# Optimization experiments

Hardware: AMD Instinct MI355X
Metric: run time of the kernel (lower is better)

The kernel has to match this reference:

```python
import jax, jax.numpy as jnp
from jax import lax
import numpy as np

B, T = 64, 256
V_CHAR, V_DICT = 8000, 30
CHAR_E, POS_E = 256, 128
POS_H, MAIN_H = 256, 512      # bidirectional output dims
LBL = 18 + 2                  # label_size + START/STOP


def _lstm_dir(x, maskf, Wih, Whh, b):
    """Unidirectional LSTM with PyTorch gate order (i,f,g,o); masked steps hold state, outputs zeroed at pads."""
    Bb = x.shape[0]
    H = Whh.shape[1]
    def step(carry, inp):
        h, c = carry
        xt, mt = inp  # xt [B,D], mt [B,1]
        g = xt @ Wih.T + h @ Whh.T + b
        i, f, gg, o = jnp.split(g, 4, axis=-1)
        c2 = jax.nn.sigmoid(f) * c + jax.nn.sigmoid(i) * jnp.tanh(gg)
        h2 = jax.nn.sigmoid(o) * jnp.tanh(c2)
        h = mt * h2 + (1.0 - mt) * h
        c = mt * c2 + (1.0 - mt) * c
        return (h, c), h * mt
    init = (jnp.zeros((Bb, H), x.dtype), jnp.zeros((Bb, H), x.dtype))
    _, ys = lax.scan(step, init, (x.transpose(1, 0, 2), maskf.T[:, :, None]))
    return ys.transpose(1, 0, 2)  # [B,T,H]


def _bilstm(x, lengths, maskf, Wih_f, Whh_f, b_f, Wih_b, Whh_b, b_b):
    """Packed-sequence BiLSTM: backward direction runs over each sequence reversed by its own length."""
    Tt = x.shape[1]
    out_f = _lstm_dir(x, maskf, Wih_f, Whh_f, b_f)
    rev_idx = jnp.clip(lengths[:, None] - 1 - jnp.arange(Tt)[None, :], 0, Tt - 1)  # [B,T]
    x_rev = jnp.take_along_axis(x, rev_idx[:, :, None], axis=1)
    out_b_rev = _lstm_dir(x_rev, maskf, Wih_b, Whh_b, b_b)
    out_b = jnp.take_along_axis(out_b_rev, rev_idx[:, :, None], axis=1) * maskf[:, :, None]
    return jnp.concatenate([out_f, out_b], axis=-1)


def _viterbi(emit, mask, trans):
    """CRF Viterbi decode. emit [B,T,L], mask [B,T] bool, trans [L,L] (trans[i,j]=score i->j); START=L-2, STOP=L-1."""
    Bb, Tt, L = emit.shape
    START, STOP = L - 2, L - 1
    alpha0 = trans[START][None, :] + emit[:, 0]  # [B,L]
    ident = jnp.arange(L)[None, :]
    def step(alpha, inp):
        e_t, m_t = inp  # [B,L], [B,1]
        scores = alpha[:, :, None] + trans[None, :, :]  # [B,L_prev,L_cur]
        bp = jnp.argmax(scores, axis=1)
        new = jnp.max(scores, axis=1) + e_t
        alpha = jnp.where(m_t, new, alpha)
        bp = jnp.where(m_t, bp, ident)
        return alpha, bp
    alpha, bps = lax.scan(step, alpha0, (emit[:, 1:].transpose(1, 0, 2), mask[:, 1:].T[:, :, None]))
    final = alpha + trans[:, STOP][None, :]
    last_tag = jnp.argmax(final, axis=1)          # [B]
    path_score = jnp.max(final, axis=1)           # [B]
    def back(tag, bp_t):
        prev = jnp.take_along_axis(bp_t, tag[:, None], axis=1)[:, 0]
        return prev, tag
    first_tag, tags_rest = lax.scan(back, last_tag, bps, reverse=True)  # tags_rest [T-1,B]
    tags = jnp.concatenate([first_tag[:, None], tags_rest.T], axis=1)   # [B,T]
    return path_score, tags * mask.astype(tags.dtype)


def setup_inputs() -> dict:
    key = jax.random.key(0)
    ks = jax.random.split(key, 24)
    char_inputs = jax.random.randint(ks[0], (B, T), 0, V_CHAR)
    pos_inputs = jax.random.randint(ks[1], (B, T), 0, V_DICT)
    tag_inputs = jax.random.randint(ks[2], (B, T), 0, V_DICT)
    lengths = jnp.sort(jax.random.randint(ks[3], (B,), T // 2, T + 1))[::-1]
    lengths = lengths.at[0].set(T)  # pack_padded requires descending lengths; max len defines T
    mask = jnp.arange(T)[None, :] < lengths[:, None]
    s = 0.08
    def rn(k, shape):
        return jax.random.normal(k, shape, jnp.float32) * s
    Hp, Hm = POS_H // 2, MAIN_H // 2
    Dm = CHAR_E + POS_E + POS_H
    return dict(
        char_inputs=char_inputs, pos_inputs=pos_inputs, tag_inputs=tag_inputs,
        lengths=lengths, mask=mask,
        char_emb=rn(ks[4], (V_CHAR, CHAR_E)),
        pos_emb=rn(ks[5], (V_DICT, POS_E)),
        tag_pos_emb=rn(ks[6], (V_DICT, POS_E)),
        pWih_f=rn(ks[7], (4 * Hp, POS_E)), pWhh_f=rn(ks[8], (4 * Hp, Hp)), pb_f=rn(ks[9], (4 * Hp,)),
        pWih_b=rn(ks[10], (4 * Hp, POS_E)), pWhh_b=rn(ks[11], (4 * Hp, Hp)), pb_b=rn(ks[12], (4 * Hp,)),
        mWih_f=rn(ks[13], (4 * Hm, Dm)), mWhh_f=rn(ks[14], (4 * Hm, Hm)), mb_f=rn(ks[15], (4 * Hm,)),
        mWih_b=rn(ks[16], (4 * Hm, Dm)), mWhh_b=rn(ks[17], (4 * Hm, Hm)), mb_b=rn(ks[18], (4 * Hm,)),
        W_out=rn(ks[19], (LBL, MAIN_H)), b_out=rn(ks[20], (LBL,)),
        trans=rn(ks[21], (LBL, LBL)),
    )


def reference(char_inputs, pos_inputs, tag_inputs, lengths, mask,
              char_emb, pos_emb, tag_pos_emb,
              pWih_f, pWhh_f, pb_f, pWih_b, pWhh_b, pb_b,
              mWih_f, mWhh_f, mb_f, mWih_b, mWhh_b, mb_b,
              W_out, b_out, trans):
    maskf = mask.astype(jnp.float32)
    # PosBiLSTM: embeds tag_inputs with its own pos table, runs BiLSTM (dropout is identity at eval)
    tag_embs = tag_pos_emb[tag_inputs]
    pos_lstm_out = _bilstm(tag_embs, lengths, maskf, pWih_f, pWhh_f, pb_f, pWih_b, pWhh_b, pb_b)
    # Main BiLSTM over [char_emb | pos_emb | pos_lstm_out]
    emb = jnp.concatenate([char_emb[char_inputs], pos_emb[pos_inputs], pos_lstm_out], axis=-1)
    lstm_out = _bilstm(emb, lengths, maskf, mWih_f, mWhh_f, mb_f, mWih_b, mWhh_b, mb_b)
    emit = lstm_out @ W_out.T + b_out  # [B,T,LBL]
    _, tag_seq = _viterbi(emit, mask, trans)
    return tag_seq
```

## Files before the change

### kernel.cpp

```cpp
#include <hip/hip_runtime.h>
#include <hip/hip_bf16.h>
#include <math.h>


#define Bsz 64
#define Tsz 256
#define NROW 16384

__device__ __forceinline__ float sigm(float x) { return 1.f / (1.f + expf(-x)); }

#define PIN4(v) asm volatile("" : "+v"((v).x), "+v"((v).y), "+v"((v).z), "+v"((v).w))

typedef float f32x4 __attribute__((ext_vector_type(4)));
typedef short short8 __attribute__((ext_vector_type(8)));

__device__ __forceinline__ void bf16split(float f, ushort& h, ushort& l) {
  unsigned u = __float_as_uint(f);
  unsigned hh = (u + 0x7FFFu + ((u >> 16) & 1u)) >> 16;
  h = (ushort)hh;
  float hf = __uint_as_float(hh << 16);
  unsigned v = __float_as_uint(f - hf);
  l = (ushort)((v + 0x7FFFu + ((v >> 16) & 1u)) >> 16);
}

__global__ __launch_bounds__(256) void gather_kernel(
    const int* __restrict__ ci, const int* __restrict__ pi, const int* __restrict__ ti,
    const float* __restrict__ ce, const float* __restrict__ pe, const float* __restrict__ te,
    float* __restrict__ tbuf, float* __restrict__ emb) {
  int gid = blockIdx.x * 256 + threadIdx.x;
  int m = gid >> 7, s = gid & 127;
  if (s < 32) {
    ((float4*)&tbuf[(size_t)m * 128])[s] = ((const float4*)&te[(size_t)ti[m] * 128])[s];
  } else if (s < 96) {
    ((float4*)&emb[(size_t)m * 640])[s - 32] = ((const float4*)&ce[(size_t)ci[m] * 256])[s - 32];
  } else {
    ((float4*)&emb[(size_t)m * 640 + 256])[s - 96] = ((const float4*)&pe[(size_t)pi[m] * 128])[s - 96];
  }
}

__global__ __launch_bounds__(256) void gemm_mfma(
    const float* __restrict__ A, int lda,
    const float* __restrict__ W, int ldb,
    const float* __restrict__ bias,
    float* __restrict__ C, int ldc, int col0, int K) {
  __shared__ __align__(16) ushort Ah[128][40];
  __shared__ __align__(16) ushort Al[128][40];
  __shared__ __align__(16) ushort Bh[128][40];
  __shared__ __align__(16) ushort Bl[128][40];
  const int tid = threadIdx.x;
  const int lane = tid & 63, wv = tid >> 6;
  const int l15 = lane & 15, l8 = (lane >> 4) * 8;
  const int m0 = blockIdx.y * 128, n0 = blockIdx.x * 128;

  f32x4 acc[2][8] = {};
  for (int k0 = 0; k0 < K; k0 += 32) {
#pragma unroll
    for (int rr = 0; rr < 4; ++rr) {
      int fi = tid + rr * 256;
      int row = fi >> 3, q4 = (fi & 7) * 4;
      float4 av = *(const float4*)&A[(size_t)(m0 + row) * lda + k0 + q4];
      ushort4 h, l;
      bf16split(av.x, h.x, l.x); bf16split(av.y, h.y, l.y);
      bf16split(av.z, h.z, l.z); bf16split(av.w, h.w, l.w);
      *(ushort4*)&Ah[row][q4] = h; *(ushort4*)&Al[row][q4] = l;
      float4 bv = *(const float4*)&W[(size_t)(n0 + row) * ldb + k0 + q4];
      bf16split(bv.x, h.x, l.x); bf16split(bv.y, h.y, l.y);
      bf16split(bv.z, h.z, l.z); bf16split(bv.w, h.w, l.w);
      *(ushort4*)&Bh[row][q4] = h; *(ushort4*)&Bl[row][q4] = l;
    }
    __syncthreads();
    short8 aH[2], aL[2];
#pragma unroll
    for (int f = 0; f < 2; ++f) {
      aH[f] = *(const short8*)&Ah[wv * 32 + f * 16 + l15][l8];
      aL[f] = *(const short8*)&Al[wv * 32 + f * 16 + l15][l8];
    }
#pragma unroll
    for (int fc = 0; fc < 8; ++fc) {
      short8 bH = *(const short8*)&Bh[fc * 16 + l15][l8];
      short8 bL = *(const short8*)&Bl[fc * 16 + l15][l8];
#pragma unroll
      for (int f = 0; f < 2; ++f) {
        acc[f][fc] = __builtin_amdgcn_mfma_f32_16x16x32_bf16(aH[f], bH, acc[f][fc], 0, 0, 0);
        acc[f][fc] = __builtin_amdgcn_mfma_f32_16x16x32_bf16(aH[f], bL, acc[f][fc], 0, 0, 0);
        acc[f][fc] = __builtin_amdgcn_mfma_f32_16x16x32_bf16(aL[f], bH, acc[f][fc], 0, 0, 0);
      }
    }
    __syncthreads();
  }
  const int l4 = lane >> 4;
#pragma unroll
  for (int f = 0; f < 2; ++f)
#pragma unroll
    for (int fc = 0; fc < 8; ++fc) {
      int col = fc * 16 + l15;
      float bs = bias[n0 + col];
#pragma unroll
      for (int q = 0; q < 4; ++q) {
        size_t row = m0 + wv * 32 + f * 16 + l4 * 4 + q;
        C[row * ldc + col0 + n0 + col] = acc[f][fc][q] + bs;
      }
    }
}

__global__ __launch_bounds__(512, 2) void pos_rec(
    const int* __restrict__ lengths, const float* __restrict__ gpos,
    const float* __restrict__ Wf, const float* __restrict__ Wb,
    float* __restrict__ emb) {
  const int blk = blockIdx.x;
  const int b = blk >> 1, dir = blk & 1;
  const int j = threadIdx.x;
  const int gc = j >> 7;
  const int len = lengths[b];
  const float* W = dir ? Wb : Wf;
  __shared__ __align__(16) float h[128];
  __shared__ float gbuf[512];
  float4 w4[32];
#pragma unroll
  for (int i = 0; i < 32; ++i) w4[i] = *(const float4*)&W[(size_t)j * 128 + i * 4];
#pragma unroll
  for (int i = 0; i < 32; ++i) PIN4(w4[i]);
  float c = 0.f;
  if (j < 128) h[j] = 0.f;
  __syncthreads();
  int idx0 = dir ? (len - 1) : 0;
  float gcur = gpos[((size_t)(b * Tsz + idx0)) * 1024 + dir * 512 + j];
  for (int t = 0; t < len; ++t) {
    const int idx = dir ? (len - 1 - t) : t;
    const int tn = (t + 1 < len) ? t + 1 : t;
    const int idxn = dir ? (len - 1 - tn) : tn;
    float gnext = gpos[((size_t)(b * Tsz + idxn)) * 1024 + dir * 512 + j];
    float acc = gcur;
    const float4* h4 = (const float4*)h;
#pragma unroll
    for (int i = 0; i < 32; ++i) {
      float4 hh = h4[i];
      acc = fmaf(hh.x, w4[i].x, acc); acc = fmaf(hh.y, w4[i].y, acc);
      acc = fmaf(hh.z, w4[i].z, acc); acc = fmaf(hh.w, w4[i].w, acc);
    }
    gbuf[j] = (gc == 2) ? tanhf(acc) : sigm(acc);
    __syncthreads();
    if (j < 128) {
      float si = gbuf[j], sf = gbuf[128 + j], tg = gbuf[256 + j], so = gbuf[384 + j];
      c = sf * c + si * tg;
      float hn = so * tanhf(c);
      h[j] = hn;
      emb[((size_t)(b * Tsz + idx)) * 640 + 384 + dir * 128 + j] = hn;
    }
    __syncthreads();
    gcur = gnext;
  }
}

#define MR_VF4 40
#define MR_LF4 19
#define MR_TF4 5
#define HX_STRIDE 256
__global__ __launch_bounds__(512, 2) void main_rec(
    const int* __restrict__ lengths, const float* __restrict__ gmain,
    const float* __restrict__ Wf, const float* __restrict__ Wb,
    float* __restrict__ lstm_out, unsigned long long* __restrict__ hx) {
  extern __shared__ float smem[];
  float4* wl  = (float4*)smem;
  float* hbuf = smem + MR_LF4 * 512 * 4;
  float* gbuf = hbuf + 256;

  const int blk = blockIdx.x;
  const int b = blk >> 2, dir = (blk >> 1) & 1, half = blk & 1;
  const int j = threadIdx.x;
  const int gc = j >> 7, ul = j & 127;
  const int r = gc * 256 + half * 128 + ul;
  const int len = lengths[b];
  const float* Wr = (dir ? Wb : Wf) + (size_t)r * 256;

  float4 wv[MR_VF4];
#pragma unroll
  for (int i = 0; i < MR_VF4; ++i) wv[i] = *(const float4*)&Wr[i * 4];
#pragma unroll
  for (int i = 0; i < MR_VF4; ++i) PIN4(wv[i]);
#pragma unroll
  for (int i = 0; i < MR_LF4; ++i) wl[i * 512 + j] = *(const float4*)&Wr[(MR_VF4 + i) * 4];

  unsigned long long* selfD = hx + (size_t)blk * HX_STRIDE;
  unsigned long long* partD = hx + (size_t)(blk ^ 1) * HX_STRIDE;
  const int obase = dir * 256 + half * 128;

  float c = 0.f;
  if (j < 256) hbuf[j] = 0.f;
  __syncthreads();

  const int idx0 = dir ? (len - 1) : 0;
  float gcur = gmain[((size_t)(b * Tsz + idx0)) * 2048 + dir * 1024 + r];
  for (int t = 0; t < len; ++t) {
    const int idx = dir ? (len - 1 - t) : t;
    const int tn = (t + 1 < len) ? t + 1 : t;
    const int idxn = dir ? (len - 1 - tn) : tn;
    float gnext = gmain[((size_t)(b * Tsz + idxn)) * 2048 + dir * 1024 + r];
    float acc = gcur;
    const float4* hb4 = (const float4*)hbuf;
#pragma unroll
    for (int i = 0; i < MR_VF4; ++i) {
      float4 hh = hb4[i], w = wv[i];
      acc = fmaf(hh.x, w.x, acc); acc = fmaf(hh.y, w.y, acc);
      acc = fmaf(hh.z, w.z, acc); acc = fmaf(hh.w, w.w, acc);
    }
#pragma unroll
    for (int i = 0; i < MR_LF4; ++i) {
      float4 hh = hb4[MR_VF4 + i], w = wl[i * 512 + j];
      acc = fmaf(hh.x, w.x, acc); acc = fmaf(hh.y, w.y, acc);
      acc = fmaf(hh.z, w.z, acc); acc = fmaf(hh.w, w.w, acc);
    }
#pragma unroll
    for (int i = 0; i < MR_TF4; ++i) {
      float4 hh = hb4[MR_VF4 + MR_LF4 + i];
      float4 w = *(const float4*)&Wr[(MR_VF4 + MR_LF4 + i) * 4];
      acc = fmaf(hh.x, w.x, acc); acc = fmaf(hh.y, w.y, acc);
      acc = fmaf(hh.z, w.z, acc); acc = fmaf(hh.w, w.w, acc);
    }
    gbuf[j] = (gc == 2) ? tanhf(acc) : sigm(acc);
    __syncthreads();
    if (j < 128) {
      float si = gbuf[ul], sf = gbuf[128 + ul], tg = gbuf[256 + ul], so = gbuf[384 + ul];
      c = sf * c + si * tg;
      float hn = so * tanhf(c);
      if (t + 1 < len) {
        union { float f; unsigned u; } cv; cv.f = hn;
        unsigned long long pk =
            ((unsigned long long)(unsigned)(t + 1) << 32) | (unsigned long long)cv.u;
        __hip_atomic_store(&selfD[(t & 1) * 128 + ul], pk,
                           __ATOMIC_RELAXED, __HIP_MEMORY_SCOPE_AGENT);
      }
      lstm_out[((size_t)(b * Tsz + idx)) * 512 + obase + ul] = hn;
      hbuf[half * 128 + ul] = hn;
      if (t + 1 < len) {
        unsigned long long pv; int guard = 0;
        for (;;) {
          pv = __hip_atomic_load(&partD[(t & 1) * 128 + ul],
                                 __ATOMIC_RELAXED, __HIP_MEMORY_SCOPE_AGENT);
          if ((unsigned)(pv >> 32) == (unsigned)(t + 1)) break;
          if (++guard > (1 << 22)) break;
          __builtin_amdgcn_s_sleep(1);
        }
        union { unsigned u; float f; } hv; hv.u = (unsigned)(pv & 0xffffffffull);
        hbuf[(half ^ 1) * 128 + ul] = hv.f;
      }
    }
    __syncthreads();
    gcur = gnext;
  }
}

__global__ __launch_bounds__(256) void emit_kernel(
    const float* __restrict__ lstm_out, const float* __restrict__ Wout,
    const float* __restrict__ bout, float* __restrict__ emit) {
  int gid = blockIdx.x * 256 + threadIdx.x;
  int m = gid >> 5, j = gid & 31;
  if (j >= 20) return;
  const float4* xr = (const float4*)&lstm_out[(size_t)m * 512];
  const float4* wr = (const float4*)&Wout[(size_t)j * 512];
  float acc = bout[j];
#pragma unroll 8
  for (int i = 0; i < 128; ++i) {
    float4 x = xr[i], w = wr[i];
    acc += x.x * w.x + x.y * w.y + x.z * w.z + x.w * w.w;
  }
  emit[(size_t)m * 20 + j] = acc;
}

__global__ __launch_bounds__(64) void viterbi_kernel(
    const int* __restrict__ lengths, const float* __restrict__ emit,
    const float* __restrict__ trans, int* __restrict__ out) {
  const int b = blockIdx.x, j = threadIdx.x;
  const int len = lengths[b];
  __shared__ float tr[400];
  __shared__ float alpha[20];
  __shared__ float fin[20];
  __shared__ unsigned char bp[256][20];
  for (int i = j; i < 400; i += 64) tr[i] = trans[i];
  __syncthreads();
  if (j < 20) alpha[j] = tr[18 * 20 + j] + emit[(size_t)(b * Tsz) * 20 + j];
  __syncthreads();
  for (int t = 1; t < len; ++t) {
    float best = 0.f; int bi = 0;
    if (j < 20) {
      best = alpha[0] + tr[j];
#pragma unroll
      for (int i = 1; i < 20; ++i) {
        float s = alpha[i] + tr[i * 20 + j];
        if (s > best) { best = s; bi = i; }
      }
      best += emit[((size_t)(b * Tsz + t)) * 20 + j];
    }
    __syncthreads();
    if (j < 20) { alpha[j] = best; bp[t][j] = (unsigned char)bi; }
    __syncthreads();
  }
  if (j < 20) fin[j] = alpha[j] + tr[j * 20 + 19];
  __syncthreads();
  if (j == 0) {
    float best = fin[0]; int tag = 0;
    for (int i = 1; i < 20; ++i) if (fin[i] > best) { best = fin[i]; tag = i; }
    out[b * Tsz + len - 1] = tag;
    for (int t = len - 1; t >= 1; --t) { tag = bp[t][tag]; out[b * Tsz + t - 1] = tag; }
  }
  for (int t = len + j; t < Tsz; t += 64) out[b * Tsz + t] = 0;
}

extern "C" void kernel_launch(void* const* d_in, const int* in_sizes, int n_in,
                              void* d_out, int out_size, void* d_ws, size_t ws_size,
                              hipStream_t stream) {
  const int*   char_in = (const int*)d_in[0];
  const int*   pos_in  = (const int*)d_in[1];
  const int*   tag_in  = (const int*)d_in[2];
  const int*   lengths = (const int*)d_in[3];
  const float* ce      = (const float*)d_in[5];
  const float* pe      = (const float*)d_in[6];
  const float* te      = (const float*)d_in[7];
  const float* pWih_f  = (const float*)d_in[8];
  const float* pWhh_f  = (const float*)d_in[9];
  const float* pb_f    = (const float*)d_in[10];
  const float* pWih_b  = (const float*)d_in[11];
  const float* pWhh_b  = (const float*)d_in[12];
  const float* pb_b    = (const float*)d_in[13];
  const float* mWih_f  = (const float*)d_in[14];
  const float* mWhh_f  = (const float*)d_in[15];
  const float* mb_f    = (const float*)d_in[16];
  const float* mWih_b  = (const float*)d_in[17];
  const float* mWhh_b  = (const float*)d_in[18];
  const float* mb_b    = (const float*)d_in[19];
  const float* W_out   = (const float*)d_in[20];
  const float* b_out   = (const float*)d_in[21];
  const float* trans   = (const float*)d_in[22];

  float* ws = (float*)d_ws;
  const size_t EMB     = 0;
  const size_t LSTMOUT = EMB + (size_t)NROW * 640;
  const size_t EMIT    = LSTMOUT + (size_t)NROW * 512;
  const size_t HX      = EMIT + (size_t)NROW * 20;
  const size_t TBUF    = HX + 256 * HX_STRIDE * 2;
  const size_t GPOS    = TBUF + (size_t)NROW * 128;
  const size_t GMAIN   = TBUF;

  hipMemsetAsync(ws + HX, 0, 256 * HX_STRIDE * sizeof(unsigned long long), stream);

  gather_kernel<<<8192, 256, 0, stream>>>(char_in, pos_in, tag_in, ce, pe, te,
                                          ws + TBUF, ws + EMB);

  gemm_mfma<<<dim3(4, 128), 256, 0, stream>>>(ws + TBUF, 128, pWih_f, 128, pb_f,
                                              ws + GPOS, 1024, 0, 128);
  gemm_mfma<<<dim3(4, 128), 256, 0, stream>>>(ws + TBUF, 128, pWih_b, 128, pb_b,
                                              ws + GPOS, 1024, 512, 128);

  pos_rec<<<128, 512, 0, stream>>>(lengths, ws + GPOS, pWhh_f, pWhh_b, ws + EMB);

  gemm_mfma<<<dim3(8, 128), 256, 0, stream>>>(ws + EMB, 640, mWih_f, 640, mb_f,
                                              ws + GMAIN, 2048, 0, 640);
  gemm_mfma<<<dim3(8, 128), 256, 0, stream>>>(ws + EMB, 640, mWih_b, 640, mb_b,
                                              ws + GMAIN, 2048, 1024, 640);

  const int SMEM = MR_LF4 * 512 * 16 + 256 * 4 + 512 * 4;
  hipFuncSetAttribute((const void*)main_rec,
                      hipFuncAttributeMaxDynamicSharedMemorySize, SMEM);
  main_rec<<<256, 512, SMEM, stream>>>(lengths, ws + GMAIN, mWhh_f, mWhh_b,
                                       ws + LSTMOUT, (unsigned long long*)(ws + HX));

  emit_kernel<<<2048, 256, 0, stream>>>(ws + LSTMOUT, W_out, b_out, ws + EMIT);

  viterbi_kernel<<<64, 64, 0, stream>>>(lengths, ws + EMIT, trans, (int*)d_out);
}
```

Measured before the change: 1.303 ms.

## Pre-split operands to bf16 hi/lo and use larger prefetched bf16x3 GEMM tiles

Weights are pre-split into bf16 high/low halves by a new kernel, and the gather and pos recurrence now write activations directly as bf16 hi/lo pairs. The GEMM no longer converts fp32 in its inner loop and loads bf16 tiles straight to shared memory. It uses 512x128 tiles with register prefetch of the next k-slice, and fuses the forward and backward weight GEMMs into one launch. This removes repeated split arithmetic and halves launches, at the cost of an extra split pass, a much larger workspace layout, and a much larger shared-memory tile.

```diff
diff --git a/kernel.cpp b/kernel.cpp
--- a/kernel.cpp
+++ b/kernel.cpp
@@ -13,100 +13,150 @@
 
 typedef float f32x4 __attribute__((ext_vector_type(4)));
 typedef short short8 __attribute__((ext_vector_type(8)));
-
-__device__ __forceinline__ void bf16split(float f, ushort& h, ushort& l) {
+typedef unsigned short u16;
+typedef u16 u16x8 __attribute__((ext_vector_type(8)));
+
+__device__ __forceinline__ void bf16split(float f, u16& h, u16& l) {
   unsigned u = __float_as_uint(f);
   unsigned hh = (u + 0x7FFFu + ((u >> 16) & 1u)) >> 16;
-  h = (ushort)hh;
+  h = (u16)hh;
   float hf = __uint_as_float(hh << 16);
   unsigned v = __float_as_uint(f - hf);
-  l = (ushort)((v + 0x7FFFu + ((v >> 16) & 1u)) >> 16);
+  l = (u16)((v + 0x7FFFu + ((v >> 16) & 1u)) >> 16);
+}
+
+__global__ __launch_bounds__(256) void wsplit4(
+    const float* __restrict__ s0, u16* __restrict__ h0, u16* __restrict__ l0, int n0,
+    const float* __restrict__ s1, u16* __restrict__ h1, u16* __restrict__ l1, int n1,
+    const float* __restrict__ s2, u16* __restrict__ h2, u16* __restrict__ l2, int n2,
+    const float* __restrict__ s3, u16* __restrict__ h3, u16* __restrict__ l3, int n3) {
+  int i = (blockIdx.x * 256 + threadIdx.x) * 4;
+  const float* s; u16 *h, *l;
+  if (i < n0) { s = s0; h = h0; l = l0; }
+  else if ((i -= n0) < n1) { s = s1; h = h1; l = l1; }
+  else if ((i -= n1) < n2) { s = s2; h = h2; l = l2; }
+  else if ((i -= n2) < n3) { s = s3; h = h3; l = l3; }
+  else return;
+  float4 v = *(const float4*)&s[i];
+  ushort4 hh, ll;
+  bf16split(v.x, hh.x, ll.x); bf16split(v.y, hh.y, ll.y);
+  bf16split(v.z, hh.z, ll.z); bf16split(v.w, hh.w, ll.w);
+  *(ushort4*)&h[i] = hh; *(ushort4*)&l[i] = ll;
 }
 
 __global__ __launch_bounds__(256) void gather_kernel(
     const int* __restrict__ ci, const int* __restrict__ pi, const int* __restrict__ ti,
     const float* __restrict__ ce, const float* __restrict__ pe, const float* __restrict__ te,
-    float* __restrict__ tbuf, float* __restrict__ emb) {
+    u16* __restrict__ tbh, u16* __restrict__ tbl,
+    u16* __restrict__ emh, u16* __restrict__ eml) {
   int gid = blockIdx.x * 256 + threadIdx.x;
   int m = gid >> 7, s = gid & 127;
+  float4 v; size_t off; u16 *ph, *pl;
   if (s < 32) {
-    ((float4*)&tbuf[(size_t)m * 128])[s] = ((const float4*)&te[(size_t)ti[m] * 128])[s];
+    v = ((const float4*)&te[(size_t)ti[m] * 128])[s];
+    off = (size_t)m * 128 + s * 4; ph = tbh; pl = tbl;
   } else if (s < 96) {
-    ((float4*)&emb[(size_t)m * 640])[s - 32] = ((const float4*)&ce[(size_t)ci[m] * 256])[s - 32];
+    v = ((const float4*)&ce[(size_t)ci[m] * 256])[s - 32];
+    off = (size_t)m * 640 + (s - 32) * 4; ph = emh; pl = eml;
   } else {
-    ((float4*)&emb[(size_t)m * 640 + 256])[s - 96] = ((const float4*)&pe[(size_t)pi[m] * 128])[s - 96];
-  }
-}
-
-__global__ __launch_bounds__(256) void gemm_mfma(
-    const float* __restrict__ A, int lda,
-    const float* __restrict__ W, int ldb,
-    const float* __restrict__ bias,
-    float* __restrict__ C, int ldc, int col0, int K) {
-  __shared__ __align__(16) ushort Ah[128][40];
-  __shared__ __align__(16) ushort Al[128][40];
-  __shared__ __align__(16) ushort Bh[128][40];
-  __shared__ __align__(16) ushort Bl[128][40];
+    v = ((const float4*)&pe[(size_t)pi[m] * 128])[s - 96];
+    off = (size_t)m * 640 + 256 + (s - 96) * 4; ph = emh; pl = eml;
+  }
+  ushort4 h, l;
+  bf16split(v.x, h.x, l.x); bf16split(v.y, h.y, l.y);
+  bf16split(v.z, h.z, l.z); bf16split(v.w, h.w, l.w);
+  *(ushort4*)&ph[off] = h; *(ushort4*)&pl[off] = l;
+}
+
+#define GTM 512
+#define GTN 128
+__global__ __launch_bounds__(512) void gemm_bf16x3(
+    const u16* __restrict__ Ah, const u16* __restrict__ Al,
+    const u16* __restrict__ Wh, const u16* __restrict__ Wl,
+    const float* __restrict__ biasF, const float* __restrict__ biasB,
+    float* __restrict__ C, int ldc, int K, int NhB) {
+  extern __shared__ u16 us[];
+  u16* As_h = us;
+  u16* As_l = us + 512 * 40;
+  u16* Ws_h = us + 2 * 512 * 40;
+  u16* Ws_l = us + 2 * 512 * 40 + 128 * 40;
   const int tid = threadIdx.x;
   const int lane = tid & 63, wv = tid >> 6;
-  const int l15 = lane & 15, l8 = (lane >> 4) * 8;
-  const int m0 = blockIdx.y * 128, n0 = blockIdx.x * 128;
-
-  f32x4 acc[2][8] = {};
+  const int l15 = lane & 15, l8 = (lane >> 4) * 8, l4 = lane >> 4;
+  const int m0 = blockIdx.y * GTM;
+  const int n0 = blockIdx.x * GTN;
+  const u16* WhS = Wh + (size_t)n0 * K;
+  const u16* WlS = Wl + (size_t)n0 * K;
+  const float* bias = (blockIdx.x < (unsigned)NhB) ? (biasF + n0)
+                                                   : (biasB + (n0 - NhB * GTN));
+  const int arow = tid >> 2, aq = (tid & 3) * 8;
+
+  u16x8 rA[4][2], rW[2];
+#define LOAD_TILES(k0)                                                         \
+  {                                                                            \
+    _Pragma("unroll")                                                          \
+    for (int r = 0; r < 4; ++r) {                                              \
+      int row = arow + r * 128;                                                \
+      rA[r][0] = *(const u16x8*)&Ah[(size_t)(m0 + row) * K + (k0) + aq];       \
+      rA[r][1] = *(const u16x8*)&Al[(size_t)(m0 + row) * K + (k0) + aq];       \
+    }                                                                          \
+    rW[0] = *(const u16x8*)&WhS[(size_t)arow * K + (k0) + aq];                 \
+    rW[1] = *(const u16x8*)&WlS[(size_t)arow * K + (k0) + aq];                 \
+  }
+
+  f32x4 acc[4][8] = {};
+  LOAD_TILES(0);
   for (int k0 = 0; k0 < K; k0 += 32) {
 #pragma unroll
-    for (int rr = 0; rr < 4; ++rr) {
-      int fi = tid + rr * 256;
-      int row = fi >> 3, q4 = (fi & 7) * 4;
-      float4 av = *(const float4*)&A[(size_t)(m0 + row) * lda + k0 + q4];
-      ushort4 h, l;
-      bf16split(av.x, h.x, l.x); bf16split(av.y, h.y, l.y);
-      bf16split(av.z, h.z, l.z); bf16split(av.w, h.w, l.w);
-      *(ushort4*)&Ah[row][q4] = h; *(ushort4*)&Al[row][q4] = l;
-      float4 bv = *(const float4*)&W[(size_t)(n0 + row) * ldb + k0 + q4];
-      bf16split(bv.x, h.x, l.x); bf16split(bv.y, h.y, l.y);
-      bf16split(bv.z, h.z, l.z); bf16split(bv.w, h.w, l.w);
-      *(ushort4*)&Bh[row][q4] = h; *(ushort4*)&Bl[row][q4] = l;
-    }
-    __syncthreads();
-    short8 aH[2], aL[2];
-#pragma unroll
-    for (int f = 0; f < 2; ++f) {
-      aH[f] = *(const short8*)&Ah[wv * 32 + f * 16 + l15][l8];
-      aL[f] = *(const short8*)&Al[wv * 32 + f * 16 + l15][l8];
-    }
-#pragma unroll
-    for (int fc = 0; fc < 8; ++fc) {
-      short8 bH = *(const short8*)&Bh[fc * 16 + l15][l8];
-      short8 bL = *(const short8*)&Bl[fc * 16 + l15][l8];
-#pragma unroll
-      for (int f = 0; f < 2; ++f) {
-        acc[f][fc] = __builtin_amdgcn_mfma_f32_16x16x32_bf16(aH[f], bH, acc[f][fc], 0, 0, 0);
-        acc[f][fc] = __builtin_amdgcn_mfma_f32_16x16x32_bf16(aH[f], bL, acc[f][fc], 0, 0, 0);
-        acc[f][fc] = __builtin_amdgcn_mfma_f32_16x16x32_bf16(aL[f], bH, acc[f][fc], 0, 0, 0);
+    for (int r = 0; r < 4; ++r) {
+      int row = arow + r * 128;
+      *(u16x8*)&As_h[row * 40 + aq] = rA[r][0];
+      *(u16x8*)&As_l[row * 40 + aq] = rA[r][1];
+    }
+    if (arow < 128) {
+      *(u16x8*)&Ws_h[arow * 40 + aq] = rW[0];
+      *(u16x8*)&Ws_l[arow * 40 + aq] = rW[1];
+    }
+    __syncthreads();
+    if (k0 + 32 < K) LOAD_TILES(k0 + 32);
+    short8 aH[4], aL[4];
+#pragma unroll
+    for (int fr = 0; fr < 4; ++fr) {
+      aH[fr] = *(const short8*)&As_h[(wv * 64 + fr * 16 + l15) * 40 + l8];
+      aL[fr] = *(const short8*)&As_l[(wv * 64 + fr * 16 + l15) * 40 + l8];
+    }
+#pragma unroll
+    for (int cf = 0; cf < 8; ++cf) {
+      short8 bH = *(const short8*)&Ws_h[(cf * 16 + l15) * 40 + l8];
+      short8 bL = *(const short8*)&Ws_l[(cf * 16 + l15) * 40 + l8];
+#pragma unroll
+      for (int fr = 0; fr < 4; ++fr) {
+        acc[fr][cf] = __builtin_amdgcn_mfma_f32_16x16x32_bf16(aH[fr], bH, acc[fr][cf], 0, 0, 0);
+        acc[fr][cf] = __builtin_amdgcn_mfma_f32_16x16x32_bf16(aH[fr], bL, acc[fr][cf], 0, 0, 0);
+        acc[fr][cf] = __builtin_amdgcn_mfma_f32_16x16x32_bf16(aL[fr], bH, acc[fr][cf], 0, 0, 0);
       }
     }
     __syncthreads();
   }
-  const int l4 = lane >> 4;
-#pragma unroll
-  for (int f = 0; f < 2; ++f)
-#pragma unroll
-    for (int fc = 0; fc < 8; ++fc) {
-      int col = fc * 16 + l15;
-      float bs = bias[n0 + col];
+#pragma unroll
+  for (int fr = 0; fr < 4; ++fr)
+#pragma unroll
+    for (int cf = 0; cf < 8; ++cf) {
+      int col = cf * 16 + l15;
+      float bs = bias[col];
 #pragma unroll
       for (int q = 0; q < 4; ++q) {
-        size_t row = m0 + wv * 32 + f * 16 + l4 * 4 + q;
-        C[row * ldc + col0 + n0 + col] = acc[f][fc][q] + bs;
+        size_t row = m0 + wv * 64 + fr * 16 + l4 * 4 + q;
+        C[row * ldc + n0 + col] = acc[fr][cf][q] + bs;
       }
     }
+#undef LOAD_TILES
 }
 
 __global__ __launch_bounds__(512, 2) void pos_rec(
     const int* __restrict__ lengths, const float* __restrict__ gpos,
     const float* __restrict__ Wf, const float* __restrict__ Wb,
-    float* __restrict__ emb) {
+    u16* __restrict__ emh, u16* __restrict__ eml) {
   const int blk = blockIdx.x;
   const int b = blk >> 1, dir = blk & 1;
   const int j = threadIdx.x;
@@ -145,7 +195,9 @@
       c = sf * c + si * tg;
       float hn = so * tanhf(c);
       h[j] = hn;
-      emb[((size_t)(b * Tsz + idx)) * 640 + 384 + dir * 128 + j] = hn;
+      u16 hh2, hl2; bf16split(hn, hh2, hl2);
+      size_t eo = ((size_t)(b * Tsz + idx)) * 640 + 384 + dir * 128 + j;
+      emh[eo] = hh2; eml[eo] = hl2;
     }
     __syncthreads();
     gcur = gnext;
@@ -333,30 +385,48 @@
   const float* trans   = (const float*)d_in[22];
 
   float* ws = (float*)d_ws;
-  const size_t EMB     = 0;
-  const size_t LSTMOUT = EMB + (size_t)NROW * 640;
-  const size_t EMIT    = LSTMOUT + (size_t)NROW * 512;
-  const size_t HX      = EMIT + (size_t)NROW * 20;
-  const size_t TBUF    = HX + 256 * HX_STRIDE * 2;
-  const size_t GPOS    = TBUF + (size_t)NROW * 128;
-  const size_t GMAIN   = TBUF;
-
-  hipMemsetAsync(ws + HX, 0, 256 * HX_STRIDE * sizeof(unsigned long long), stream);
+  const size_t WPH     = 0;
+  const size_t WPL     = 65536;
+  const size_t WMH     = 131072;
+  const size_t WML     = 786432;
+  const size_t EMH     = 1441792;
+  const size_t EML     = 6684672;
+  const size_t TBH     = 11927552;
+  const size_t TBL     = 12976128;
+  const size_t GPOS    = 14024704;
+  const size_t GMAIN   = 11927552;
+  const size_t LSTMOUT = 1441792;
+  const size_t EMIT    = 9830400;
+  const size_t HX      = 45481984;
+
+  hipMemsetAsync(ws + HX, 0, HX_STRIDE * 256 * sizeof(unsigned long long), stream);
+
+  wsplit4<<<1408, 256, 0, stream>>>(
+      pWih_f, (u16*)(ws + WPH),          (u16*)(ws + WPL),          65536,
+      pWih_b, (u16*)(ws + WPH) + 65536,  (u16*)(ws + WPL) + 65536,  65536,
+      mWih_f, (u16*)(ws + WMH),          (u16*)(ws + WML),          655360,
+      mWih_b, (u16*)(ws + WMH) + 655360, (u16*)(ws + WML) + 655360, 655360);
 
   gather_kernel<<<8192, 256, 0, stream>>>(char_in, pos_in, tag_in, ce, pe, te,
-                                          ws + TBUF, ws + EMB);
-
-  gemm_mfma<<<dim3(4, 128), 256, 0, stream>>>(ws + TBUF, 128, pWih_f, 128, pb_f,
-                                              ws + GPOS, 1024, 0, 128);
-  gemm_mfma<<<dim3(4, 128), 256, 0, stream>>>(ws + TBUF, 128, pWih_b, 128, pb_b,
-                                              ws + GPOS, 1024, 512, 128);
-
-  pos_rec<<<128, 512, 0, stream>>>(lengths, ws + GPOS, pWhh_f, pWhh_b, ws + EMB);
-
-  gemm_mfma<<<dim3(8, 128), 256, 0, stream>>>(ws + EMB, 640, mWih_f, 640, mb_f,
-                                              ws + GMAIN, 2048, 0, 640);
-  gemm_mfma<<<dim3(8, 128), 256, 0, stream>>>(ws + EMB, 640, mWih_b, 640, mb_b,
-                                              ws + GMAIN, 2048, 1024, 640);
+                                          (u16*)(ws + TBH), (u16*)(ws + TBL),
+                                          (u16*)(ws + EMH), (u16*)(ws + EML));
+
+  const int GSMEM = (2 * 512 * 40 + 2 * 128 * 40) * 2;
+  hipFuncSetAttribute((const void*)gemm_bf16x3,
+                      hipFuncAttributeMaxDynamicSharedMemorySize, GSMEM);
+
+  gemm_bf16x3<<<dim3(8, 32), 512, GSMEM, stream>>>(
+      (u16*)(ws + TBH), (u16*)(ws + TBL),
+      (u16*)(ws + WPH), (u16*)(ws + WPL),
+      pb_f, pb_b, ws + GPOS, 1024, 128, 4);
+
+  pos_rec<<<128, 512, 0, stream>>>(lengths, ws + GPOS, pWhh_f, pWhh_b,
+                                   (u16*)(ws + EMH), (u16*)(ws + EML));
+
+  gemm_bf16x3<<<dim3(16, 32), 512, GSMEM, stream>>>(
+      (u16*)(ws + EMH), (u16*)(ws + EML),
+      (u16*)(ws + WMH), (u16*)(ws + WML),
+      mb_f, mb_b, ws + GMAIN, 2048, 640, 8);
 
   const int SMEM = MR_LF4 * 512 * 16 + 256 * 4 + 512 * 4;
   hipFuncSetAttribute((const void*)main_rec,
```

Result: faster. 1.266 ms (-2.8%).
